# Kernel optimization log

Measured on AMD Instinct MI355X. Metric: run time of the kernel, lower is better.

Reference implementation:

```python
import jax, jax.numpy as jnp
import numpy as np

T, B, I = 512, 64, 768
H, L = 768, 2


def setup_inputs() -> dict:
    key = jax.random.key(0)
    ks = jax.random.split(key, 8)
    s = 1.0 / np.sqrt(H)
    return {
        "event_seq": jax.random.normal(ks[0], (T, B, I), jnp.float32),
        "h0": jax.random.normal(ks[1], (L, B, H), jnp.float32),
        "c0": jax.random.normal(ks[2], (L, B, H), jnp.float32),
        "W_ih": jax.random.uniform(ks[3], (L, 4 * H, I), jnp.float32, -s, s),
        "W_hh": jax.random.uniform(ks[4], (L, 4 * H, H), jnp.float32, -s, s),
        "b_ih": jax.random.uniform(ks[5], (L, 4 * H), jnp.float32, -s, s),
        "b_hh": jax.random.uniform(ks[6], (L, 4 * H), jnp.float32, -s, s),
        "length": jax.random.randint(ks[7], (B,), 1, T + 1, jnp.int32),
    }


def reference(event_seq, h0, c0, W_ih, W_hh, b_ih, b_hh, length):
    # event_seq: [T, B, I]; h0/c0: [L, B, H]; W_ih/W_hh: [L, 4H, *]
    ts = jnp.arange(event_seq.shape[0])

    def step(carry, xt_t):
        h, c = carry                      # [L, B, H] each
        x_t, t = xt_t
        mask = (t < length).astype(x_t.dtype)[:, None]  # [B, 1]
        x = x_t
        hs, cs = [], []
        for l in range(L):
            gates = x @ W_ih[l].T + b_ih[l] + h[l] @ W_hh[l].T + b_hh[l]
            i_g, f_g, g_g, o_g = jnp.split(gates, 4, axis=-1)  # torch LSTMCell order
            c_new = jax.nn.sigmoid(f_g) * c[l] + jax.nn.sigmoid(i_g) * jnp.tanh(g_g)
            h_new = jax.nn.sigmoid(o_g) * jnp.tanh(c_new)
            h_new = mask * h_new + (1.0 - mask) * h[l]
            c_new = mask * c_new + (1.0 - mask) * c[l]
            hs.append(h_new)
            cs.append(c_new)
            x = h_new  # dropout=0 -> identity between layers
        h = jnp.stack(hs)
        c = jnp.stack(cs)
        return (h, c), h

    (h_f, c_f), out = jax.lax.scan(step, (h0, c0), (event_seq, ts))
    # out: [T, L, B, H] -> [T, B, L, H] (matches torch.stack(..., dim=2))
    out = out.transpose(0, 2, 1, 3)
    return out, h_f, c_f
```

## Files before the change

### kernel.cpp

```cpp
#include <hip/hip_runtime.h>

typedef unsigned short u16;
typedef unsigned int u32;
typedef unsigned long long u64;
typedef __attribute__((ext_vector_type(8))) short short8;
typedef __attribute__((ext_vector_type(4))) float f32x4;

#define T_STEPS 512
#define HF_OFF 50331648UL

#define BCAT_OFF  18874368UL
#define HB0_OFF   18898944UL
#define HB1_OFF   (HB0_OFF + 32UL*98304UL)
#define FLG_OFF   (HB1_OFF + 4UL*98304UL)

__device__ __forceinline__ u16 f2bf(float f) {
  union { float f; unsigned u; } v; v.f = f;
  unsigned r = (v.u + 0x7FFFu + ((v.u >> 16) & 1u)) >> 16;
  return (u16)r;
}

__device__ __forceinline__ short8 pack8(float4 f0, float4 f1) {
  short8 v;
  v[0]=(short)f2bf(f0.x); v[1]=(short)f2bf(f0.y); v[2]=(short)f2bf(f0.z); v[3]=(short)f2bf(f0.w);
  v[4]=(short)f2bf(f1.x); v[5]=(short)f2bf(f1.y); v[6]=(short)f2bf(f1.z); v[7]=(short)f2bf(f1.w);
  return v;
}

__device__ __forceinline__ float sigm(float x) { return 1.0f / (1.0f + __expf(-x)); }
__device__ __forceinline__ float tanh_f(float x) { return 1.0f - 2.0f / (__expf(2.0f * x) + 1.0f); }

__device__ __forceinline__ short8 load_sc_b128(const void* p) {
  short8 r;
  asm volatile("global_load_dwordx4 %0, %1, off sc0 sc1" : "=&v"(r) : "v"((u64)p));
  return r;
}
__device__ __forceinline__ u32 load_sc_b32(const u32* p) {
  u32 r;
  asm volatile("global_load_dword %0, %1, off sc0 sc1\n\ts_waitcnt vmcnt(0)"
               : "=&v"(r) : "v"((u64)p) : "memory");
  return r;
}
__device__ __forceinline__ void store_sc_b32(u32* p, u32 v) {
  asm volatile("global_store_dword %0, %1, off sc0 sc1" :: "v"((u64)p), "v"(v) : "memory");
}

__device__ __forceinline__ void poll1(const u32* base, int own) {
  const int ln = threadIdx.x & 63;
  for (;;) {
    u32 f = load_sc_b32(base + ln);
    if (own >= 0 && ln == own) f = 1u;
    if (__all(f != 0)) break;
    __builtin_amdgcn_s_sleep(1);
  }
}

__global__ void prep_weights(const float* __restrict__ Wih, const float* __restrict__ Whh,
                             u16* __restrict__ Wr) {
  int idx = blockIdx.x * blockDim.x + threadIdx.x;
  if (idx >= 2 * 3072 * 192) return;
  int r = idx / 192;
  int kc = (idx - r * 192) * 8;
  int l = r / 3072;
  int rr = r - l * 3072;
  int j = rr >> 2, g = rr & 3;
  int srow = l * 3072 + g * 768 + j;
  const float* src = (kc < 768) ? (Wih + (size_t)srow * 768 + kc)
                                : (Whh + (size_t)srow * 768 + (kc - 768));
  float4 f0 = *(const float4*)src;
  float4 f1 = *(const float4*)(src + 4);
  *(short8*)(Wr + (size_t)r * 1536 + kc) = pack8(f0, f1);
}

__global__ void prep_misc(const float* __restrict__ h0, const float* __restrict__ bih,
                          const float* __restrict__ bhh, u16* __restrict__ hb0,
                          u16* __restrict__ hb1, float* __restrict__ bcat,
                          u32* __restrict__ flags) {
  int idx = blockIdx.x * blockDim.x + threadIdx.x;
  if (idx < 131584) {
    flags[idx] = (((idx >> 7) % 514) == 0) ? 1u : 0u;
  } else if (idx < 131584 + 98304) {
    int r = idx - 131584;
    int l = r / 49152, o = r - l * 49152;
    u16 v = f2bf(h0[r]);
    if (l == 0) hb0[o] = v; else hb1[o] = v;
  } else if (idx < 131584 + 98304 + 6144) {
    int q = idx - (131584 + 98304);
    int l = q / 3072, rr = q - l * 3072;
    int j = rr >> 2, g = rr & 3;
    int s = l * 3072 + g * 768 + j;
    bcat[q] = bih[s] + bhh[s];
  }
}

__global__ void __launch_bounds__(512, 2)
lstm_dataflow(const float* __restrict__ x, const float* __restrict__ h0,
              const float* __restrict__ c0, const int* __restrict__ len,
              const u16* __restrict__ Wr, const float* __restrict__ bcat,
              u16* __restrict__ hb0, u16* __restrict__ hb1,
              u32* __restrict__ flags, float* __restrict__ out) {
  __shared__ u16 lA[32 * 1536];
  __shared__ float pP[8 * 48 * 32];
  __shared__ u16 lH[32 * 12];

  const int tid = threadIdx.x;
  const int wv = tid >> 6;
  const int ln = tid & 63;
  const int wg = blockIdx.x;
  const int layer = wg >> 7;
  const int rg = (wg >> 6) & 1;
  const int cg = wg & 63;
  const int n0 = cg * 48;
  const int row = tid >> 4;
  const int uu = tid & 15;

  short8 bfr[3][6];
  {
    const u16* wbase = Wr + (size_t)(layer * 3072 + n0) * 1536;
#pragma unroll
    for (int ct = 0; ct < 3; ++ct)
#pragma unroll
      for (int ks = 0; ks < 6; ++ks) {
        int col = ct * 16 + (ln & 15);
        int k = wv * 192 + ks * 32 + ((ln >> 4) << 3);
        bfr[ct][ks] = *(const short8*)(wbase + (size_t)col * 1536 + k);
      }
  }
  float bc[3] = {0.f, 0.f, 0.f};
  if (wv == 0) {
#pragma unroll
    for (int ct = 0; ct < 3; ++ct)
      bc[ct] = bcat[layer * 3072 + n0 + ct * 16 + (ln & 15)];
  }
  const int cellb = tid / 12, cellj = tid - (tid / 12) * 12;
  float cReg = 0.f, hKeep = 0.f; int lenB = 0;
  if (tid < 384) {
    int b = rg * 32 + cellb, j = cg * 12 + cellj;
    cReg = c0[(size_t)(layer * 64 + b) * 768 + j];
    hKeep = h0[(size_t)(layer * 64 + b) * 768 + j];
    lenB = len[b];
  }

  char* lAb = (char*)lA;

  for (int t = 0; t < T_STEPS; ++t) {
    if (layer == 0) {
      const float* xb = x + ((size_t)t * 64 + rg * 32 + row) * 768;
#pragma unroll
      for (int i = 0; i < 6; ++i) {
        int unit = uu + i * 16;
        int kel = (unit * 8) ^ ((row & 7) << 3);
        float4 f0 = *(const float4*)(xb + kel);
        float4 f1 = *(const float4*)(xb + kel + 4);
        *(short8*)(lAb + row * 3072 + unit * 16) = pack8(f0, f1);
      }
      poll1(flags + ((size_t)(0 * 514 + t) * 2 + rg) * 64, cg);
      if ((t & 7) == 0 && t >= 8)
        poll1(flags + ((size_t)(1 * 514 + (t - 8)) * 2 + rg) * 64, -1);
      const u16* hp = hb0 + (size_t)(t & 31) * 49152 + (size_t)(rg * 32 + row) * 768;
      short8 hv[6];
#pragma unroll
      for (int i = 0; i < 6; ++i) {
        int unit = uu + (i + 6) * 16;
        int kel = (unit * 8) ^ ((row & 7) << 3);
        hv[i] = load_sc_b128(hp + (kel - 768));
      }
      __builtin_amdgcn_sched_barrier(0);
      asm volatile("s_waitcnt vmcnt(0)" ::: "memory");
      __builtin_amdgcn_sched_barrier(0);
#pragma unroll
      for (int i = 0; i < 6; ++i) {
        int unit = uu + (i + 6) * 16;
        *(short8*)(lAb + row * 3072 + unit * 16) = hv[i];
      }
    } else {
      poll1(flags + ((size_t)(0 * 514 + (t + 1)) * 2 + rg) * 64, -1);
      const u16* hc = hb0 + (size_t)((t + 1) & 31) * 49152 + (size_t)(rg * 32 + row) * 768;
      short8 hv[12];
#pragma unroll
      for (int i = 0; i < 6; ++i) {
        int unit = uu + i * 16;
        int kel = (unit * 8) ^ ((row & 7) << 3);
        hv[i] = load_sc_b128(hc + kel);
      }
      poll1(flags + ((size_t)(1 * 514 + t) * 2 + rg) * 64, cg);
      const u16* hp = hb1 + (size_t)(t & 3) * 49152 + (size_t)(rg * 32 + row) * 768;
#pragma unroll
      for (int i = 0; i < 6; ++i) {
        int unit = uu + (i + 6) * 16;
        int kel = (unit * 8) ^ ((row & 7) << 3);
        hv[6 + i] = load_sc_b128(hp + (kel - 768));
      }
      __builtin_amdgcn_sched_barrier(0);
      asm volatile("s_waitcnt vmcnt(0)" ::: "memory");
      __builtin_amdgcn_sched_barrier(0);
#pragma unroll
      for (int i = 0; i < 12; ++i) {
        int unit = uu + i * 16;
        *(short8*)(lAb + row * 3072 + unit * 16) = hv[i];
      }
    }
    __syncthreads();

    f32x4 acc[2][3];
#pragma unroll
    for (int rt = 0; rt < 2; ++rt)
#pragma unroll
      for (int ct = 0; ct < 3; ++ct) {
        float b0 = (wv == 0) ? bc[ct] : 0.f;
        acc[rt][ct] = (f32x4){b0, b0, b0, b0};
      }
#pragma unroll
    for (int ks = 0; ks < 6; ++ks) {
      int kb = (wv * 192 + ks * 32 + ((ln >> 4) << 3)) * 2;
#pragma unroll
      for (int rt = 0; rt < 2; ++rt) {
        int arow = rt * 16 + (ln & 15);
        short8 a = *(const short8*)(lAb + arow * 3072 + (kb ^ ((arow & 7) << 4)));
#pragma unroll
        for (int ct = 0; ct < 3; ++ct)
          acc[rt][ct] = __builtin_amdgcn_mfma_f32_16x16x32_bf16(a, bfr[ct][ks], acc[rt][ct], 0, 0, 0);
      }
    }
#pragma unroll
    for (int rt = 0; rt < 2; ++rt)
#pragma unroll
      for (int ct = 0; ct < 3; ++ct) {
        int col = ct * 16 + (ln & 15);
        int q0 = rt * 16 + ((ln >> 4) << 2);
        *(f32x4*)((char*)pP + wv * 6144 + col * 128 + ((q0 * 4) ^ ((col & 7) << 4))) = acc[rt][ct];
      }
    __syncthreads();

    if (tid < 384) {
      float g4[4];
#pragma unroll
      for (int g = 0; g < 4; ++g) {
        int col = cellj * 4 + g;
        float s = 0.f;
#pragma unroll
        for (int w = 0; w < 8; ++w)
          s += *(const float*)((const char*)pP + w * 6144 + col * 128 + ((cellb * 4) ^ ((col & 7) << 4)));
        g4[g] = s;
      }
      float cn = sigm(g4[1]) * cReg + sigm(g4[0]) * tanh_f(g4[2]);
      float hn = sigm(g4[3]) * tanh_f(cn);
      const bool act = t < lenB;
      float hm = act ? hn : hKeep;
      float cm = act ? cn : cReg;
      hKeep = hm; cReg = cm;
      int bglob = rg * 32 + cellb, j = cg * 12 + cellj;
      out[((size_t)(t * 64 + bglob) * 2 + layer) * 768 + j] = hm;
      lH[cellb * 12 + cellj] = f2bf(hm);
    }
    __syncthreads();

    if (wv == 0) {
      u16* hout = (layer == 0) ? hb0 + (size_t)((t + 1) & 31) * 49152
                               : hb1 + (size_t)((t + 1) & 3) * 49152;
      const u32* lH32 = (const u32*)lH;
#pragma unroll
      for (int it = 0; it < 3; ++it) {
        int idx = ln + it * 64;
        int r = idx / 6, w = idx - (idx / 6) * 6;
        u32 v = lH32[r * 6 + w];
        store_sc_b32((u32*)((char*)hout + (size_t)(rg * 32 + r) * 1536 + cg * 24 + w * 4), v);
      }
      asm volatile("s_waitcnt vmcnt(0)" ::: "memory");
      if (ln == 0)
        store_sc_b32(flags + ((size_t)(layer * 514 + (t + 1)) * 2 + rg) * 64 + cg, 1u);
    }
  }

  if (tid < 384) {
    int b = rg * 32 + cellb, j = cg * 12 + cellj;
    float* hf = out + HF_OFF;
    float* cf = out + HF_OFF + 98304;
    hf[(size_t)(layer * 64 + b) * 768 + j] = hKeep;
    cf[(size_t)(layer * 64 + b) * 768 + j] = cReg;
  }
}

extern "C" void kernel_launch(void* const* d_in, const int* in_sizes, int n_in,
                              void* d_out, int out_size, void* d_ws, size_t ws_size,
                              hipStream_t stream) {
  const float* x   = (const float*)d_in[0];
  const float* h0  = (const float*)d_in[1];
  const float* c0  = (const float*)d_in[2];
  const float* Wih = (const float*)d_in[3];
  const float* Whh = (const float*)d_in[4];
  const float* bih = (const float*)d_in[5];
  const float* bhh = (const float*)d_in[6];
  const int*   len = (const int*)d_in[7];
  float* out = (float*)d_out;

  u16*   Wr    = (u16*)d_ws;
  float* bcat  = (float*)((char*)d_ws + BCAT_OFF);
  u16*   hb0   = (u16*)((char*)d_ws + HB0_OFF);
  u16*   hb1   = (u16*)((char*)d_ws + HB1_OFF);
  u32*   flags = (u32*)((char*)d_ws + FLG_OFF);

  {
    const int units = 2 * 3072 * 192;
    prep_weights<<<(units + 255) / 256, 256, 0, stream>>>(Wih, Whh, Wr);
    const int n2 = 131584 + 98304 + 6144;
    prep_misc<<<(n2 + 255) / 256, 256, 0, stream>>>(h0, bih, bhh, hb0, hb1, bcat, flags);
  }

  void* args[] = { (void*)&x, (void*)&h0, (void*)&c0, (void*)&len,
                   (void*)&Wr, (void*)&bcat, (void*)&hb0, (void*)&hb1,
                   (void*)&flags, (void*)&out };
  hipLaunchCooperativeKernel((const void*)lstm_dataflow, dim3(256), dim3(512),
                             args, 0, stream);
}
```

Measured before the change: 4.707 ms.

## Precompute input-projection MFMA for the next step off the recurrent critical path

Splits the per-step GEMM into an input part (x or layer-0 h) and a recurrent part, with separate register-resident weight slices. The input contribution for step t+1 is computed and staged right after the cell update of step t, so only the recurrent half waits on the cross-block flag. Waves are re-split into 4 K-slices by 2 row tiles, so the LDS reduction shrinks to 4 partials per gate. Cells now write bf16 h straight to global and set per-wave byte flags that consumers check against a 64-bit mask. Holding both weight halves in registers doubles weight register pressure under the existing launch bounds, which could cause spills.

```diff
diff --git a/kernel.cpp b/kernel.cpp
--- a/kernel.cpp
+++ b/kernel.cpp
@@ -8,11 +8,13 @@
 
 #define T_STEPS 512
 #define HF_OFF 50331648UL
-
-#define BCAT_OFF  18874368UL
-#define HB0_OFF   18898944UL
-#define HB1_OFF   (HB0_OFF + 32UL*98304UL)
-#define FLG_OFF   (HB1_OFF + 4UL*98304UL)
+#define SLOT 49152
+
+#define BCAT_OFF 18874368UL
+#define HB0_OFF  18898944UL
+#define HB1_OFF  (HB0_OFF + 32UL*98304UL)
+#define FLG_OFF  (HB1_OFF + 4UL*98304UL)
+#define READYMASK 0x0000010101010101ULL
 
 __device__ __forceinline__ u16 f2bf(float f) {
   union { float f; unsigned u; } v; v.f = f;
@@ -35,23 +37,55 @@
   asm volatile("global_load_dwordx4 %0, %1, off sc0 sc1" : "=&v"(r) : "v"((u64)p));
   return r;
 }
-__device__ __forceinline__ u32 load_sc_b32(const u32* p) {
-  u32 r;
-  asm volatile("global_load_dword %0, %1, off sc0 sc1\n\ts_waitcnt vmcnt(0)"
+__device__ __forceinline__ u64 load_sc_b64w(const void* p) {
+  u64 r;
+  asm volatile("global_load_dwordx2 %0, %1, off sc0 sc1\n\ts_waitcnt vmcnt(0)"
                : "=&v"(r) : "v"((u64)p) : "memory");
   return r;
 }
-__device__ __forceinline__ void store_sc_b32(u32* p, u32 v) {
-  asm volatile("global_store_dword %0, %1, off sc0 sc1" :: "v"((u64)p), "v"(v) : "memory");
-}
-
-__device__ __forceinline__ void poll1(const u32* base, int own) {
+__device__ __forceinline__ void store_sc_b16(void* p, u32 v) {
+  asm volatile("global_store_short %0, %1, off sc0 sc1" :: "v"((u64)p), "v"(v) : "memory");
+}
+__device__ __forceinline__ void store_sc_b8(void* p, u32 v) {
+  asm volatile("global_store_byte %0, %1, off sc0 sc1" :: "v"((u64)p), "v"(v) : "memory");
+}
+
+__device__ __forceinline__ void pollu(const u64* base, int own) {
   const int ln = threadIdx.x & 63;
   for (;;) {
-    u32 f = load_sc_b32(base + ln);
-    if (own >= 0 && ln == own) f = 1u;
-    if (__all(f != 0)) break;
+    u64 f = load_sc_b64w(base + ln);
+    if (ln == own) f = READYMASK;
+    if (__all(f == READYMASK)) break;
     __builtin_amdgcn_s_sleep(1);
+  }
+}
+
+__device__ __forceinline__ void stage_u16(u16* dstL, const u16* srcRow, int row, int uu) {
+  short8 hv[6];
+#pragma unroll
+  for (int i = 0; i < 6; ++i) {
+    int unit = uu + i * 16;
+    int kel = (unit * 8) ^ ((row & 7) << 3);
+    hv[i] = load_sc_b128(srcRow + kel);
+  }
+  __builtin_amdgcn_sched_barrier(0);
+  asm volatile("s_waitcnt vmcnt(0)" ::: "memory");
+  __builtin_amdgcn_sched_barrier(0);
+#pragma unroll
+  for (int i = 0; i < 6; ++i) {
+    int unit = uu + i * 16;
+    *(short8*)((char*)dstL + row * 1536 + unit * 16) = hv[i];
+  }
+}
+
+__device__ __forceinline__ void stage_xf(u16* dstL, const float* srcRow, int row, int uu) {
+#pragma unroll
+  for (int i = 0; i < 6; ++i) {
+    int unit = uu + i * 16;
+    int kel = (unit * 8) ^ ((row & 7) << 3);
+    float4 f0 = *(const float4*)(srcRow + kel);
+    float4 f1 = *(const float4*)(srcRow + kel + 4);
+    *(short8*)((char*)dstL + row * 1536 + unit * 16) = pack8(f0, f1);
   }
 }
 
@@ -75,10 +109,10 @@
 __global__ void prep_misc(const float* __restrict__ h0, const float* __restrict__ bih,
                           const float* __restrict__ bhh, u16* __restrict__ hb0,
                           u16* __restrict__ hb1, float* __restrict__ bcat,
-                          u32* __restrict__ flags) {
+                          u64* __restrict__ flags) {
   int idx = blockIdx.x * blockDim.x + threadIdx.x;
   if (idx < 131584) {
-    flags[idx] = (((idx >> 7) % 514) == 0) ? 1u : 0u;
+    flags[idx] = (((idx >> 7) % 514) == 0) ? READYMASK : 0ULL;
   } else if (idx < 131584 + 98304) {
     int r = idx - 131584;
     int l = r / 49152, o = r - l * 49152;
@@ -98,14 +132,16 @@
               const float* __restrict__ c0, const int* __restrict__ len,
               const u16* __restrict__ Wr, const float* __restrict__ bcat,
               u16* __restrict__ hb0, u16* __restrict__ hb1,
-              u32* __restrict__ flags, float* __restrict__ out) {
-  __shared__ u16 lA[32 * 1536];
-  __shared__ float pP[8 * 48 * 32];
-  __shared__ u16 lH[32 * 12];
+              u64* __restrict__ flags, float* __restrict__ out) {
+  __shared__ u16 lAh[32 * 768];
+  __shared__ u16 lAx[32 * 768];
+  __shared__ float pP[48 * 32 * 4];
 
   const int tid = threadIdx.x;
   const int wv = tid >> 6;
   const int ln = tid & 63;
+  const int ks = wv & 3;
+  const int rt = wv >> 2;
   const int wg = blockIdx.x;
   const int layer = wg >> 7;
   const int rg = (wg >> 6) & 1;
@@ -113,21 +149,23 @@
   const int n0 = cg * 48;
   const int row = tid >> 4;
   const int uu = tid & 15;
-
-  short8 bfr[3][6];
+  const int arow = rt * 16 + (ln & 15);
+
+  short8 Wx[3][6], Wh[3][6];
   {
     const u16* wbase = Wr + (size_t)(layer * 3072 + n0) * 1536;
 #pragma unroll
     for (int ct = 0; ct < 3; ++ct)
 #pragma unroll
-      for (int ks = 0; ks < 6; ++ks) {
+      for (int kst = 0; kst < 6; ++kst) {
         int col = ct * 16 + (ln & 15);
-        int k = wv * 192 + ks * 32 + ((ln >> 4) << 3);
-        bfr[ct][ks] = *(const short8*)(wbase + (size_t)col * 1536 + k);
+        int k = ks * 192 + kst * 32 + ((ln >> 4) << 3);
+        Wx[ct][kst] = *(const short8*)(wbase + (size_t)col * 1536 + k);
+        Wh[ct][kst] = *(const short8*)(wbase + (size_t)col * 1536 + 768 + k);
       }
   }
   float bc[3] = {0.f, 0.f, 0.f};
-  if (wv == 0) {
+  if (ks == 0) {
 #pragma unroll
     for (int ct = 0; ct < 3; ++ct)
       bc[ct] = bcat[layer * 3072 + n0 + ct * 16 + (ln & 15)];
@@ -141,95 +179,67 @@
     lenB = len[b];
   }
 
-  char* lAb = (char*)lA;
+  f32x4 acc_x[3];
+  auto run_xmfma = [&]() {
+#pragma unroll
+    for (int ct = 0; ct < 3; ++ct)
+      acc_x[ct] = (ks == 0) ? (f32x4){bc[ct], bc[ct], bc[ct], bc[ct]}
+                            : (f32x4){0.f, 0.f, 0.f, 0.f};
+#pragma unroll
+    for (int kst = 0; kst < 6; ++kst) {
+      int kel = ks * 192 + kst * 32 + ((ln >> 4) << 3);
+      short8 a = *(const short8*)((const char*)lAx + arow * 1536 + ((kel * 2) ^ ((arow & 7) << 4)));
+#pragma unroll
+      for (int ct = 0; ct < 3; ++ct)
+        acc_x[ct] = __builtin_amdgcn_mfma_f32_16x16x32_bf16(a, Wx[ct][kst], acc_x[ct], 0, 0, 0);
+    }
+  };
+  auto stage_x = [&](int u) {
+    if (layer == 0) {
+      stage_xf(lAx, x + ((size_t)u * 64 + rg * 32 + row) * 768, row, uu);
+    } else {
+      pollu(flags + ((size_t)(0 * 514 + (u + 1)) * 2 + rg) * 64, -1);
+      stage_u16(lAx, hb0 + (size_t)((u + 1) & 31) * SLOT + (size_t)(rg * 32 + row) * 768, row, uu);
+    }
+  };
+
+  stage_x(0);
+  __syncthreads();
+  run_xmfma();
+  __syncthreads();
+  stage_x(1);
 
   for (int t = 0; t < T_STEPS; ++t) {
-    if (layer == 0) {
-      const float* xb = x + ((size_t)t * 64 + rg * 32 + row) * 768;
-#pragma unroll
-      for (int i = 0; i < 6; ++i) {
-        int unit = uu + i * 16;
-        int kel = (unit * 8) ^ ((row & 7) << 3);
-        float4 f0 = *(const float4*)(xb + kel);
-        float4 f1 = *(const float4*)(xb + kel + 4);
-        *(short8*)(lAb + row * 3072 + unit * 16) = pack8(f0, f1);
+    pollu(flags + ((size_t)(layer * 514 + t) * 2 + rg) * 64, cg);
+    {
+      const u16* hp = (layer == 0) ? hb0 + (size_t)(t & 31) * SLOT
+                                   : hb1 + (size_t)(t & 3) * SLOT;
+      stage_u16(lAh, hp + (size_t)(rg * 32 + row) * 768, row, uu);
+    }
+    __syncthreads();
+
+    f32x4 acc[3];
+#pragma unroll
+    for (int ct = 0; ct < 3; ++ct) acc[ct] = acc_x[ct];
+#pragma unroll
+    for (int kst = 0; kst < 6; ++kst) {
+      int kel = ks * 192 + kst * 32 + ((ln >> 4) << 3);
+      short8 a = *(const short8*)((const char*)lAh + arow * 1536 + ((kel * 2) ^ ((arow & 7) << 4)));
+#pragma unroll
+      for (int ct = 0; ct < 3; ++ct)
+        acc[ct] = __builtin_amdgcn_mfma_f32_16x16x32_bf16(a, Wh[ct][kst], acc[ct], 0, 0, 0);
+    }
+
+#pragma unroll
+    for (int ct = 0; ct < 3; ++ct) {
+      int col = ct * 16 + (ln & 15);
+      int kwp = ks ^ (col & 3);
+#pragma unroll
+      for (int i = 0; i < 4; ++i) {
+        int bloc = rt * 16 + ((ln >> 4) << 2) + i;
+        pP[col * 128 + ((bloc ^ (col & 7)) << 2) + kwp] = acc[ct][i];
       }
-      poll1(flags + ((size_t)(0 * 514 + t) * 2 + rg) * 64, cg);
-      if ((t & 7) == 0 && t >= 8)
-        poll1(flags + ((size_t)(1 * 514 + (t - 8)) * 2 + rg) * 64, -1);
-      const u16* hp = hb0 + (size_t)(t & 31) * 49152 + (size_t)(rg * 32 + row) * 768;
-      short8 hv[6];
-#pragma unroll
-      for (int i = 0; i < 6; ++i) {
-        int unit = uu + (i + 6) * 16;
-        int kel = (unit * 8) ^ ((row & 7) << 3);
-        hv[i] = load_sc_b128(hp + (kel - 768));
-      }
-      __builtin_amdgcn_sched_barrier(0);
-      asm volatile("s_waitcnt vmcnt(0)" ::: "memory");
-      __builtin_amdgcn_sched_barrier(0);
-#pragma unroll
-      for (int i = 0; i < 6; ++i) {
-        int unit = uu + (i + 6) * 16;
-        *(short8*)(lAb + row * 3072 + unit * 16) = hv[i];
-      }
-    } else {
-      poll1(flags + ((size_t)(0 * 514 + (t + 1)) * 2 + rg) * 64, -1);
-      const u16* hc = hb0 + (size_t)((t + 1) & 31) * 49152 + (size_t)(rg * 32 + row) * 768;
-      short8 hv[12];
-#pragma unroll
-      for (int i = 0; i < 6; ++i) {
-        int unit = uu + i * 16;
-        int kel = (unit * 8) ^ ((row & 7) << 3);
-        hv[i] = load_sc_b128(hc + kel);
-      }
-      poll1(flags + ((size_t)(1 * 514 + t) * 2 + rg) * 64, cg);
-      const u16* hp = hb1 + (size_t)(t & 3) * 49152 + (size_t)(rg * 32 + row) * 768;
-#pragma unroll
-      for (int i = 0; i < 6; ++i) {
-        int unit = uu + (i + 6) * 16;
-        int kel = (unit * 8) ^ ((row & 7) << 3);
-        hv[6 + i] = load_sc_b128(hp + (kel - 768));
-      }
-      __builtin_amdgcn_sched_barrier(0);
-      asm volatile("s_waitcnt vmcnt(0)" ::: "memory");
-      __builtin_amdgcn_sched_barrier(0);
-#pragma unroll
-      for (int i = 0; i < 12; ++i) {
-        int unit = uu + i * 16;
-        *(short8*)(lAb + row * 3072 + unit * 16) = hv[i];
-      }
-    }
-    __syncthreads();
-
-    f32x4 acc[2][3];
-#pragma unroll
-    for (int rt = 0; rt < 2; ++rt)
-#pragma unroll
-      for (int ct = 0; ct < 3; ++ct) {
-        float b0 = (wv == 0) ? bc[ct] : 0.f;
-        acc[rt][ct] = (f32x4){b0, b0, b0, b0};
-      }
-#pragma unroll
-    for (int ks = 0; ks < 6; ++ks) {
-      int kb = (wv * 192 + ks * 32 + ((ln >> 4) << 3)) * 2;
-#pragma unroll
-      for (int rt = 0; rt < 2; ++rt) {
-        int arow = rt * 16 + (ln & 15);
-        short8 a = *(const short8*)(lAb + arow * 3072 + (kb ^ ((arow & 7) << 4)));
-#pragma unroll
-        for (int ct = 0; ct < 3; ++ct)
-          acc[rt][ct] = __builtin_amdgcn_mfma_f32_16x16x32_bf16(a, bfr[ct][ks], acc[rt][ct], 0, 0, 0);
-      }
-    }
-#pragma unroll
-    for (int rt = 0; rt < 2; ++rt)
-#pragma unroll
-      for (int ct = 0; ct < 3; ++ct) {
-        int col = ct * 16 + (ln & 15);
-        int q0 = rt * 16 + ((ln >> 4) << 2);
-        *(f32x4*)((char*)pP + wv * 6144 + col * 128 + ((q0 * 4) ^ ((col & 7) << 4))) = acc[rt][ct];
-      }
+    }
     __syncthreads();
 
     if (tid < 384) {
@@ -237,11 +247,8 @@
 #pragma unroll
       for (int g = 0; g < 4; ++g) {
         int col = cellj * 4 + g;
-        float s = 0.f;
-#pragma unroll
-        for (int w = 0; w < 8; ++w)
-          s += *(const float*)((const char*)pP + w * 6144 + col * 128 + ((cellb * 4) ^ ((col & 7) << 4)));
-        g4[g] = s;
+        f32x4 v = *(const f32x4*)&pP[col * 128 + ((cellb ^ (col & 7)) << 2)];
+        g4[g] = (v[0] + v[1]) + (v[2] + v[3]);
       }
       float cn = sigm(g4[1]) * cReg + sigm(g4[0]) * tanh_f(g4[2]);
       float hn = sigm(g4[3]) * tanh_f(cn);
@@ -249,27 +256,23 @@
       float hm = act ? hn : hKeep;
       float cm = act ? cn : cReg;
       hKeep = hm; cReg = cm;
-      int bglob = rg * 32 + cellb, j = cg * 12 + cellj;
-      out[((size_t)(t * 64 + bglob) * 2 + layer) * 768 + j] = hm;
-      lH[cellb * 12 + cellj] = f2bf(hm);
-    }
+      const int bglob = rg * 32 + cellb, jglob = cg * 12 + cellj;
+      u16* hout = (layer == 0) ? hb0 + (size_t)((t + 1) & 31) * SLOT
+                               : hb1 + (size_t)((t + 1) & 3) * SLOT;
+      store_sc_b16(hout + (size_t)bglob * 768 + jglob, (u32)f2bf(hm));
+      asm volatile("s_waitcnt vmcnt(0)" ::: "memory");
+      if (ln == 0) {
+        char* fb = (char*)(flags + ((size_t)(layer * 514 + (t + 1)) * 2 + rg) * 64 + cg);
+        store_sc_b8(fb + wv, 1u);
+      }
+      out[((size_t)(t * 64 + bglob) * 2 + layer) * 768 + jglob] = hm;
+    }
+
+    if (t < T_STEPS - 1) run_xmfma();
     __syncthreads();
-
-    if (wv == 0) {
-      u16* hout = (layer == 0) ? hb0 + (size_t)((t + 1) & 31) * 49152
-                               : hb1 + (size_t)((t + 1) & 3) * 49152;
-      const u32* lH32 = (const u32*)lH;
-#pragma unroll
-      for (int it = 0; it < 3; ++it) {
-        int idx = ln + it * 64;
-        int r = idx / 6, w = idx - (idx / 6) * 6;
-        u32 v = lH32[r * 6 + w];
-        store_sc_b32((u32*)((char*)hout + (size_t)(rg * 32 + r) * 1536 + cg * 24 + w * 4), v);
-      }
-      asm volatile("s_waitcnt vmcnt(0)" ::: "memory");
-      if (ln == 0)
-        store_sc_b32(flags + ((size_t)(layer * 514 + (t + 1)) * 2 + rg) * 64 + cg, 1u);
-    }
+    if (t < T_STEPS - 2) stage_x(t + 2);
+    if (layer == 0 && (t & 7) == 0 && t >= 8)
+      pollu(flags + ((size_t)(1 * 514 + (t - 8)) * 2 + rg) * 64, -1);
   }
 
   if (tid < 384) {
@@ -298,7 +301,7 @@
   float* bcat  = (float*)((char*)d_ws + BCAT_OFF);
   u16*   hb0   = (u16*)((char*)d_ws + HB0_OFF);
   u16*   hb1   = (u16*)((char*)d_ws + HB1_OFF);
-  u32*   flags = (u32*)((char*)d_ws + FLG_OFF);
+  u64*   flags = (u64*)((char*)d_ws + FLG_OFF);
 
   {
     const int units = 2 * 3072 * 192;
```

Result: slower. 5.128 ms (+9.0%).
